# Optimization experiments

Hardware: AMD Instinct MI355X
Metric: run time of the kernel (lower is better)

The kernel has to match this reference:

```python
import jax, jax.numpy as jnp
import numpy as np

N, E, K, C, NB, G = 10000, 320000, 10, 32, 8, 8
RMAX, AVG = 5.0, 32.0
L_OF_M = np.array([0,1,1,1,2,2,2,2,2,3,3,3,3,3,3,3])
BLOCKS = [(0,1),(1,4),(4,9),(9,16)]


def _sph(u):
    # real spherical harmonics l=0..3, e3nn 'component' normalization (sum_m Y_lm^2 = 2l+1)
    x, y, z = u[:,0], u[:,1], u[:,2]
    s3=3**0.5; s5=5**0.5; s15=15**0.5; s105=105**0.5
    s35_8=(35.0/8.0)**0.5; s21_8=(21.0/8.0)**0.5; s7=7**0.5
    return jnp.stack([
        jnp.ones_like(x),
        s3*x, s3*y, s3*z,
        s15*x*y, s15*y*z, 0.5*s5*(3*z*z-1.0), s15*x*z, 0.5*s15*(x*x-y*y),
        s35_8*y*(3*x*x-y*y), s105*x*y*z, s21_8*y*(5*z*z-1.0),
        0.5*s7*z*(5*z*z-3.0), s21_8*x*(5*z*z-1.0), 0.5*s105*z*(x*x-y*y),
        s35_8*x*(x*x-3*y*y)], axis=-1)


def _radial(r):
    # Bessel basis * polynomial cutoff (p=5)
    n = jnp.arange(1, NB+1, dtype=r.dtype)
    bess = jnp.sqrt(2.0/RMAX)*jnp.sin(n*jnp.pi*r[:,None]/RMAX)/r[:,None]
    t = r/RMAX; p = 5.0
    env = 1.0 - (p+1)*(p+2)/2*t**5 + p*(p+2)*t**6 - p*(p+1)/2*t**7
    env = jnp.where(r < RMAX, env, 0.0)
    return bess*env[:,None]


def _interact(scal, ea, ef, snd, rcv, mws, Wl, n_nodes):
    h = ef
    for W in mws[:-1]:
        h = jax.nn.silu(h @ W)
    tw = (h @ mws[-1]).reshape(-1, C, 4)[:, :, L_OF_M]          # [E,C,16] per-(channel,l) tp weights
    mji = scal[snd][:, :, None] * tw * ea[:, None, :]            # per-edge CG-style tensor product
    msg = jax.ops.segment_sum(mji, rcv, num_segments=n_nodes) / AVG
    return jnp.concatenate([jnp.einsum('ncm,cd->ndm', msg[:, :, a:b], Wl[l])
                            for l, (a, b) in enumerate(BLOCKS)], axis=-1)


def _forward(positions, node_attrs, shifts, edge_index, batch, num_graphs,
             atomic_energies, W_emb, Wup1, M1a, M1b, M1c, M1d, Wl1, Wprod1,
             Wup2, M2a, M2b, M2c, M2d, Wl2, Wprod2, Wsc2, wr1, Wr2a, wr2b):
    snd, rcv = edge_index[0], edge_index[1]
    vec = positions[rcv] - positions[snd] + shifts
    r = jnp.sqrt(jnp.sum(vec*vec, -1) + 1e-12)
    ea = _sph(vec / r[:, None])           # [E,16]
    ef = _radial(r)                       # [E,8]
    nf0 = node_attrs @ W_emb              # node embedding [N,C]
    A1 = _interact(nf0 @ Wup1, ea, ef, snd, rcv, (M1a, M1b, M1c, M1d), Wl1, positions.shape[0])
    c1 = jnp.einsum('nk,kct->nct', node_attrs, Wprod1)          # element-dep product-basis coeffs
    a0 = A1[:, :, 0]
    nf1 = A1 * (c1[..., 0] + c1[..., 1]*a0 + c1[..., 2]*a0*a0)[:, :, None]  # correlation-3 product
    A2 = _interact(nf1[:, :, 0] @ Wup2, ea, ef, snd, rcv, (M2a, M2b, M2c, M2d), Wl2, positions.shape[0])
    pl = jnp.stack([jnp.sum(A2[:, :, a:b]**2, -1) for a, b in BLOCKS], -1)  # [N,C,4] invariants
    c2 = jnp.einsum('nk,kct->nct', node_attrs, Wprod2)
    nf2 = jnp.sum(c2*pl, -1) + jnp.einsum('nk,nc,kcd->nd', node_attrs, nf1[:, :, 0], Wsc2)
    e0 = node_attrs @ atomic_energies
    e1 = nf1[:, :, 0] @ wr1
    e2 = jax.nn.silu(nf2 @ Wr2a) @ wr2b
    node_energy = e0 + e1 + e2
    total = jax.ops.segment_sum(node_energy, batch, num_segments=num_graphs)
    return total, node_energy


def setup_inputs():
    key = jax.random.key(0)
    ks = jax.random.split(key, 24)
    s = 0.1
    inp = {}
    inp['positions'] = jax.random.normal(ks[0], (N, 3), jnp.float32)
    inp['node_attrs'] = jax.nn.one_hot(jax.random.randint(ks[1], (N,), 0, K), K, dtype=jnp.float32)
    inp['shifts'] = jnp.zeros((E, 3), jnp.float32)
    inp['edge_index'] = jax.random.randint(ks[2], (2, E), 0, N)
    inp['batch'] = jnp.sort(jax.random.randint(ks[3], (N,), 0, G))
    inp['num_graphs'] = G
    inp['atomic_energies'] = jax.random.normal(ks[4], (K,), jnp.float32)
    inp['W_emb'] = s*jax.random.normal(ks[5], (K, C), jnp.float32)
    inp['Wup1'] = s*jax.random.normal(ks[6], (C, C), jnp.float32)
    inp['M1a'] = s*jax.random.normal(ks[7], (NB, 64), jnp.float32)
    inp['M1b'] = s*jax.random.normal(ks[8], (64, 64), jnp.float32)
    inp['M1c'] = s*jax.random.normal(ks[9], (64, 64), jnp.float32)
    inp['M1d'] = s*jax.random.normal(ks[10], (64, C*4), jnp.float32)
    inp['Wl1'] = s*jax.random.normal(ks[11], (4, C, C), jnp.float32)
    inp['Wprod1'] = s*jax.random.normal(ks[12], (K, C, 3), jnp.float32)
    inp['Wup2'] = s*jax.random.normal(ks[13], (C, C), jnp.float32)
    inp['M2a'] = s*jax.random.normal(ks[14], (NB, 64), jnp.float32)
    inp['M2b'] = s*jax.random.normal(ks[15], (64, 64), jnp.float32)
    inp['M2c'] = s*jax.random.normal(ks[16], (64, 64), jnp.float32)
    inp['M2d'] = s*jax.random.normal(ks[17], (64, C*4), jnp.float32)
    inp['Wl2'] = s*jax.random.normal(ks[18], (4, C, C), jnp.float32)
    inp['Wprod2'] = s*jax.random.normal(ks[19], (K, C, 4), jnp.float32)
    inp['Wsc2'] = s*jax.random.normal(ks[20], (K, C, C), jnp.float32)
    inp['wr1'] = s*jax.random.normal(ks[21], (C,), jnp.float32)
    inp['Wr2a'] = s*jax.random.normal(ks[22], (C, 16), jnp.float32)
    inp['wr2b'] = s*jax.random.normal(ks[23], (16,), jnp.float32)
    return inp


def reference(positions, node_attrs, shifts, edge_index, batch, num_graphs,
              atomic_energies, W_emb, Wup1, M1a, M1b, M1c, M1d, Wl1, Wprod1,
              Wup2, M2a, M2b, M2c, M2d, Wl2, Wprod2, Wsc2, wr1, Wr2a, wr2b):
    def efn(pos):
        tot, ne = _forward(pos, node_attrs, shifts, edge_index, batch, num_graphs,
                           atomic_energies, W_emb, Wup1, M1a, M1b, M1c, M1d, Wl1, Wprod1,
                           Wup2, M2a, M2b, M2c, M2d, Wl2, Wprod2, Wsc2, wr1, Wr2a, wr2b)
        return jnp.sum(tot), (tot, ne)
    (_, (total, node_energy)), g = jax.value_and_grad(efn, has_aux=True)(positions)
    forces = -g  # forces = -dE/dpositions as in get_outputs
    return total, node_energy, forces
```

## Files before the change

### kernel.cpp

```cpp
#include <hip/hip_runtime.h>
#include <math.h>

#define NN 10000
#define NE 320000
#define KS 10
#define CC 32
#define GG 8
#define NTAB 2048
#define TROW 320
#define RMAXf 5.0f
#define AVGf 32.0f

#define OF_TAB 0
#define SZ_TAB ((NTAB + 1) * TROW)
#define OF_GEO (OF_TAB + SZ_TAB)
#define OF_SND (OF_GEO + 4 * NE)
#define OF_SPK (OF_SND + NE)
#define OF_RCSR (OF_SPK + NE)
#define OF_SC1 (OF_RCSR + NE)
#define OF_SP (OF_SC1 + KS * CC)
#define OF_RE (OF_SP + NN)
#define OF_UE (OF_RE + NE)
#define OF_GV (OF_UE + 3 * NE)
#define OF_A0 (OF_GV + 3 * NE)
#define OF_NF1 (OF_A0 + NN * CC)
#define OF_SCAL2 (OF_NF1 + NN * CC)
#define OF_NEP (OF_SCAL2 + NN * CC)
#define OF_GM2T (OF_NEP + NN)
#define OF_GNF1P (OF_GM2T + NN * CC * 16)
#define OF_GS1 (OF_GNF1P + NN * CC)
#define OF_ROWS (OF_GS1 + NN * CC)
#define OF_ELIST (OF_ROWS + NN + 1)
#define OF_DEG (OF_ELIST + NE)
#define OF_CUR (OF_DEG + NN)
#define OF_GSC2 (OF_CUR + NN)
#define OF_END (OF_GSC2 + NN * CC)

__device__ __forceinline__ int lm_of(int m) { return (m == 0) ? 0 : (m < 4) ? 1 : (m < 9) ? 2 : 3; }

__device__ __forceinline__ void sph16(float x, float y, float z, float* Y) {
    const float s3 = 1.7320508075688772f, s5 = 2.23606797749979f, s15 = 3.872983346207417f,
                s105 = 10.246950765959598f, s358 = 2.091650066335189f,
                s218 = 1.6201851746019651f, s7 = 2.6457513110645907f;
    Y[0] = 1.f;
    Y[1] = s3 * x; Y[2] = s3 * y; Y[3] = s3 * z;
    Y[4] = s15 * x * y; Y[5] = s15 * y * z; Y[6] = 0.5f * s5 * (3.f * z * z - 1.f);
    Y[7] = s15 * x * z; Y[8] = 0.5f * s15 * (x * x - y * y);
    Y[9] = s358 * y * (3.f * x * x - y * y);
    Y[10] = s105 * x * y * z;
    Y[11] = s218 * y * (5.f * z * z - 1.f);
    Y[12] = 0.5f * s7 * z * (5.f * z * z - 3.f);
    Y[13] = s218 * x * (5.f * z * z - 1.f);
    Y[14] = 0.5f * s105 * z * (x * x - y * y);
    Y[15] = s358 * x * (x * x - 3.f * y * y);
}

__device__ __forceinline__ void sph16_grad(float x, float y, float z, float* Dx, float* Dy, float* Dz) {
    const float s3 = 1.7320508075688772f, s5 = 2.23606797749979f, s15 = 3.872983346207417f,
                s105 = 10.246950765959598f, s358 = 2.091650066335189f,
                s218 = 1.6201851746019651f, s7 = 2.6457513110645907f;
    Dx[0] = 0; Dy[0] = 0; Dz[0] = 0;
    Dx[1] = s3; Dy[1] = 0; Dz[1] = 0;
    Dx[2] = 0; Dy[2] = s3; Dz[2] = 0;
    Dx[3] = 0; Dy[3] = 0; Dz[3] = s3;
    Dx[4] = s15 * y; Dy[4] = s15 * x; Dz[4] = 0;
    Dx[5] = 0; Dy[5] = s15 * z; Dz[5] = s15 * y;
    Dx[6] = 0; Dy[6] = 0; Dz[6] = 3.f * s5 * z;
    Dx[7] = s15 * z; Dy[7] = 0; Dz[7] = s15 * x;
    Dx[8] = s15 * x; Dy[8] = -s15 * y; Dz[8] = 0;
    Dx[9] = 6.f * s358 * x * y; Dy[9] = 3.f * s358 * (x * x - y * y); Dz[9] = 0;
    Dx[10] = s105 * y * z; Dy[10] = s105 * x * z; Dz[10] = s105 * x * y;
    Dx[11] = 0; Dy[11] = s218 * (5.f * z * z - 1.f); Dz[11] = 10.f * s218 * y * z;
    Dx[12] = 0; Dy[12] = 0; Dz[12] = 0.5f * s7 * (15.f * z * z - 3.f);
    Dx[13] = s218 * (5.f * z * z - 1.f); Dy[13] = 0; Dz[13] = 10.f * s218 * x * z;
    Dx[14] = s105 * x * z; Dy[14] = -s105 * y * z; Dz[14] = 0.5f * s105 * (x * x - y * y);
    Dx[15] = 3.f * s358 * (x * x - y * y); Dy[15] = -6.f * s358 * x * y; Dz[15] = 0;
}

__global__ void k_species(const float* __restrict__ na, int* __restrict__ sp) {
    int n = blockIdx.x * blockDim.x + threadIdx.x;
    if (n >= NN) return;
    int k = 0;
    for (int j = 0; j < KS; j++)
        if (na[n * KS + j] > 0.5f) k = j;
    sp[n] = k;
}

__global__ void k_scal1(const float* __restrict__ Wemb, const float* __restrict__ Wup1, float* __restrict__ st) {
    int i = threadIdx.x;
    if (i >= KS * CC) return;
    int k = i / CC, c = i % CC;
    float s = 0;
    for (int j = 0; j < CC; j++) s += Wemb[k * CC + j] * Wup1[j * CC + c];
    st[i] = s;
}

__global__ void k_table(const float* __restrict__ M1a, const float* __restrict__ M1b,
                        const float* __restrict__ M1c, const float* __restrict__ M1d,
                        const float* __restrict__ M2a, const float* __restrict__ M2b,
                        const float* __restrict__ M2c, const float* __restrict__ M2d,
                        float* __restrict__ tab) {
    const double PI = 3.14159265358979323846;
    int row = blockIdx.x;
    int j = threadIdx.x;
    __shared__ float sR[8], sdR[8];
    __shared__ float sA[64], sdA[64], sB[64], sdB[64];
    if (j < 8) {
        double r = (double)row * ((double)RMAXf / NTAB);
        if (r < 1e-6) r = 1e-6;
        double a = (double)(j + 1) * PI / (double)RMAXf;
        double env = 0.0, denv = 0.0;
        if (row < NTAB) {
            double t = r / (double)RMAXf;
            double t4 = t * t * t * t;
            env = 1.0 - 21.0 * t4 * t + 35.0 * t4 * t * t - 15.0 * t4 * t * t * t;
            denv = (-105.0 * t4 + 210.0 * t4 * t - 105.0 * t4 * t * t) / (double)RMAXf;
        }
        double pref = sqrt(2.0 / (double)RMAXf);
        double s = sin(a * r), cg = cos(a * r);
        double bess = pref * s / r;
        double dbess = pref * (a * cg / r - s / (r * r));
        sR[j] = (float)(bess * env);
        sdR[j] = (float)(dbess * env + bess * denv);
    }
    __syncthreads();
    size_t rb = (size_t)row * TROW;

    {
        float p = 0, dp = 0;
        for (int i = 0; i < 8; i++) { float w = M1a[i * 64 + j]; p += sR[i] * w; dp += sdR[i] * w; }
        float sg = 1.f / (1.f + expf(-p));
        sB[j] = p * sg; sdB[j] = dp * sg * (1.f + p * (1.f - sg));
    }
    __syncthreads();
    {
        float p = 0, dp = 0;
        for (int i = 0; i < 64; i++) { float w = M1b[i * 64 + j]; p += sB[i] * w; dp += sdB[i] * w; }
        float sg = 1.f / (1.f + expf(-p));
        sA[j] = p * sg; sdA[j] = dp * sg * (1.f + p * (1.f - sg));
    }
    __syncthreads();
    {
        float p = 0, dp = 0;
        for (int i = 0; i < 64; i++) { float w = M1c[i * 64 + j]; p += sA[i] * w; dp += sdA[i] * w; }
        float sg = 1.f / (1.f + expf(-p));
        sB[j] = p * sg; sdB[j] = dp * sg * (1.f + p * (1.f - sg));
    }
    __syncthreads();
    #pragma unroll
    for (int t2 = 0; t2 < 2; t2++) {
        int o = j + t2 * 64;
        if ((o & 3) == 0) {
            float p = 0, dp = 0;
            for (int i = 0; i < 64; i++) { float w = M1d[i * 128 + o]; p += sB[i] * w; dp += sdB[i] * w; }
            int c = o >> 2;
            tab[rb + c] = p;
            tab[rb + 32 + c] = dp;
        }
    }
    __syncthreads();

    {
        float p = 0, dp = 0;
        for (int i = 0; i < 8; i++) { float w = M2a[i * 64 + j]; p += sR[i] * w; dp += sdR[i] * w; }
        float sg = 1.f / (1.f + expf(-p));
        sB[j] = p * sg; sdB[j] = dp * sg * (1.f + p * (1.f - sg));
    }
    __syncthreads();
    {
        float p = 0, dp = 0;
        for (int i = 0; i < 64; i++) { float w = M2b[i * 64 + j]; p += sB[i] * w; dp += sdB[i] * w; }
        float sg = 1.f / (1.f + expf(-p));
        sA[j] = p * sg; sdA[j] = dp * sg * (1.f + p * (1.f - sg));
    }
    __syncthreads();
    {
        float p = 0, dp = 0;
        for (int i = 0; i < 64; i++) { float w = M2c[i * 64 + j]; p += sA[i] * w; dp += sdA[i] * w; }
        float sg = 1.f / (1.f + expf(-p));
        sB[j] = p * sg; sdB[j] = dp * sg * (1.f + p * (1.f - sg));
    }
    __syncthreads();
    #pragma unroll
    for (int t2 = 0; t2 < 2; t2++) {
        int o = j + t2 * 64;
        float p = 0, dp = 0;
        for (int i = 0; i < 64; i++) { float w = M2d[i * 128 + o]; p += sB[i] * w; dp += sdB[i] * w; }
        tab[rb + 64 + o] = p;
        tab[rb + 192 + o] = dp;
    }
}

__global__ void k_geom(const float* __restrict__ pos, const float* __restrict__ shifts,
                       const int* __restrict__ ei, float* __restrict__ re,
                       float* __restrict__ ue, int* __restrict__ deg) {
    int e = blockIdx.x * 256 + threadIdx.x;
    if (e >= NE) return;
    int s = ei[e], t = ei[NE + e];
    float vx = pos[3 * t] - pos[3 * s] + shifts[3 * e];
    float vy = pos[3 * t + 1] - pos[3 * s + 1] + shifts[3 * e + 1];
    float vz = pos[3 * t + 2] - pos[3 * s + 2] + shifts[3 * e + 2];
    float r = sqrtf(vx * vx + vy * vy + vz * vz + 1e-12f);
    float inv = 1.f / r;
    re[e] = r;
    ue[3 * e] = vx * inv;
    ue[3 * e + 1] = vy * inv;
    ue[3 * e + 2] = vz * inv;
    atomicAdd(&deg[t], 1);
}

__global__ void k_scan(const int* __restrict__ deg, int* __restrict__ rows, int* __restrict__ cur) {
    __shared__ int part[1024];
    int t = threadIdx.x;
    const int per = (NN + 1023) / 1024;
    int base = t * per;
    int s = 0;
    for (int i = 0; i < per; i++) {
        int idx = base + i;
        if (idx < NN) s += deg[idx];
    }
    part[t] = s;
    __syncthreads();
    for (int off = 1; off < 1024; off <<= 1) {
        int v = (t >= off) ? part[t - off] : 0;
        __syncthreads();
        part[t] += v;
        __syncthreads();
    }
    int run = (t == 0) ? 0 : part[t - 1];
    for (int i = 0; i < per; i++) {
        int idx = base + i;
        if (idx < NN) {
            rows[idx] = run;
            cur[idx] = run;
            run += deg[idx];
        }
    }
    if (t == 1023) rows[NN] = run;
}

__global__ void k_fill(const int* __restrict__ ei, const int* __restrict__ sp,
                       const float* __restrict__ re, const float* __restrict__ ue,
                       int* __restrict__ cur, int* __restrict__ elist,
                       int* __restrict__ snd, int* __restrict__ spk,
                       float* __restrict__ rcsr, float4* __restrict__ geo) {
    int e = blockIdx.x * 256 + threadIdx.x;
    if (e >= NE) return;
    int s = ei[e], t = ei[NE + e];
    int p = atomicAdd(&cur[t], 1);
    elist[p] = e;
    snd[p] = s;
    spk[p] = sp[s];
    rcsr[p] = re[e];
    geo[p] = make_float4(re[e], ue[3 * e], ue[3 * e + 1], ue[3 * e + 2]);
}

__global__ __launch_bounds__(256, 4)
void k_gather1(const int* __restrict__ rows, const int* __restrict__ spk,
               const float* __restrict__ rcsr, const int* __restrict__ sp,
               const float* __restrict__ sc1, const float* __restrict__ tab,
               const float* __restrict__ Wl1, const float* __restrict__ Wprod1,
               const float* __restrict__ Wup2, const float* __restrict__ wr1,
               const float* __restrict__ aE,
               float* __restrict__ a0s, float* __restrict__ nf1,
               float* __restrict__ scal2, float* __restrict__ nep) {
    __shared__ float red[4][CC];
    int wid = blockIdx.x;
    int tid = threadIdx.x;
    int wv = tid >> 6, lane = tid & 63, c = lane & 31, h = lane >> 5, hb = h << 5;
    int stream = wv * 2 + h;
    int r0 = rows[wid], dg = rows[wid + 1] - r0;
    float acc = 0.f;
    for (int j = stream; j < dg; j += 8) {
        int p = r0 + j;
        float r = rcsr[p];
        float scv = sc1[spk[p] * CC + c];
        float w1 = 0.f;
        if (r < RMAXf) {
            float tt = r * (NTAB / RMAXf);
            int i = (int)tt; if (i > NTAB - 1) i = NTAB - 1;
            float f = tt - (float)i;
            size_t b = (size_t)i * TROW + c;
            w1 = tab[b] * (1.f - f) + tab[b + TROW] * f;
        }
        acc += scv * w1;
    }
    acc += __shfl_xor(acc, 32, 64);
    if (h == 0) red[wv][c] = acc;
    __syncthreads();
    acc = red[0][c] + red[1][c] + red[2][c] + red[3][c];
    float a0 = 0.f;
    for (int d = 0; d < CC; d++) a0 += __shfl(acc, hb + d, 64) * Wl1[d * CC + c];
    a0 *= (1.f / AVGf);
    int k = sp[wid];
    const float* cp = &Wprod1[(k * CC + c) * 3];
    float nf = a0 * (cp[0] + cp[1] * a0 + cp[2] * a0 * a0);
    float s2 = 0.f;
    for (int d = 0; d < CC; d++) s2 += __shfl(nf, hb + d, 64) * Wup2[d * CC + c];
    float t1 = nf * wr1[c];
    for (int m = 16; m >= 1; m >>= 1) t1 += __shfl_xor(t1, m, 64);
    if (wv == 0 && h == 0) {
        a0s[wid * CC + c] = a0;
        nf1[wid * CC + c] = nf;
        scal2[wid * CC + c] = s2;
        if (c == 0) nep[wid] = aE[k] + t1;
    }
}

__global__ __launch_bounds__(256, 4)
void k_node2(const int* __restrict__ rows, const int* __restrict__ snd,
             const float4* __restrict__ geo, const int* __restrict__ sp,
             const float* __restrict__ scal2, const float* __restrict__ tab,
             const float* __restrict__ Wl2, const float* __restrict__ Wprod2,
             const float* __restrict__ Wsc2, const float* __restrict__ nf1,
             const float* __restrict__ Wr2a, const float* __restrict__ wr2b,
             const float* __restrict__ wr1, const float* __restrict__ nep,
             const int* __restrict__ batch,
             float* __restrict__ gm2T, float* __restrict__ gnf1p,
             float* __restrict__ out_total, float* __restrict__ out_ne) {
    __shared__ float lds[4][16 * 32];
    int wid = blockIdx.x;
    int tid = threadIdx.x;
    int wv = tid >> 6, lane = tid & 63, c = lane & 31, h = lane >> 5, hb = h << 5;
    int stream = wv * 2 + h;
    int r0 = rows[wid], dg = rows[wid + 1] - r0;

    float S2r[16];
    #pragma unroll
    for (int m = 0; m < 16; m++) S2r[m] = 0.f;
    for (int j = stream; j < dg; j += 8) {
        int p = r0 + j;
        float4 g4 = geo[p];
        float sc = scal2[snd[p] * CC + c];
        float r = g4.x;
        float scw[4] = {0, 0, 0, 0};
        if (r < RMAXf) {
            float tt = r * (NTAB / RMAXf);
            int i = (int)tt; if (i > NTAB - 1) i = NTAB - 1;
            float f = tt - (float)i;
            size_t b = (size_t)i * TROW + 64 + c * 4;
            float4 t0 = *(const float4*)&tab[b];
            float4 t1 = *(const float4*)&tab[b + TROW];
            scw[0] = sc * (t0.x + (t1.x - t0.x) * f);
            scw[1] = sc * (t0.y + (t1.y - t0.y) * f);
            scw[2] = sc * (t0.z + (t1.z - t0.z) * f);
            scw[3] = sc * (t0.w + (t1.w - t0.w) * f);
        }
        float Y[16];
        sph16(g4.y, g4.z, g4.w, Y);
        #pragma unroll
        for (int m = 0; m < 16; m++) S2r[m] += scw[lm_of(m)] * Y[m];
    }
    #pragma unroll
    for (int m = 0; m < 16; m++) S2r[m] += __shfl_xor(S2r[m], 32, 64);
    if (h == 0) {
        #pragma unroll
        for (int m = 0; m < 16; m++) lds[wv][m * 32 + c] = S2r[m];
    }
    __syncthreads();
    for (int idx = tid; idx < 512; idx += 256)
        lds[0][idx] += lds[1][idx] + lds[2][idx] + lds[3][idx];
    __syncthreads();

    int d = c;
    float A2r[16];
    #pragma unroll
    for (int m = 0; m < 16; m++) {
        const float* wl = &Wl2[lm_of(m) * CC * CC];
        float acc = 0;
        for (int cc = 0; cc < CC; cc++) acc += lds[0][m * 32 + cc] * wl[cc * CC + d];
        A2r[m] = acc * (1.f / AVGf);
    }
    float pl[4] = {0, 0, 0, 0};
    #pragma unroll
    for (int m = 0; m < 16; m++) pl[lm_of(m)] += A2r[m] * A2r[m];
    int k = sp[wid];
    const float* c2 = &Wprod2[(k * CC + d) * 4];
    float nf2 = c2[0] * pl[0] + c2[1] * pl[1] + c2[2] * pl[2] + c2[3] * pl[3];
    for (int cc = 0; cc < CC; cc++) nf2 += nf1[wid * CC + cc] * Wsc2[((size_t)k * CC + cc) * CC + d];
    int jj = d & 15;
    float zj = 0;
    for (int dd = 0; dd < CC; dd++) zj += __shfl(nf2, hb + dd, 64) * Wr2a[dd * 16 + jj];
    float sg = 1.f / (1.f + expf(-zj));
    float e2p = (d < 16) ? zj * sg * wr2b[jj] : 0.f;
    float red = e2p;
    for (int m = 16; m >= 1; m >>= 1) red += __shfl_xor(red, m, 64);
    if (wv == 0 && h == 0 && d == 0) {
        float ne = nep[wid] + red;
        out_ne[wid] = ne;
        atomicAdd(&out_total[batch[wid]], ne);
    }
    float gz = sg * (1.f + zj * (1.f - sg)) * wr2b[jj];
    float gn = 0;
    for (int j2 = 0; j2 < 16; j2++) gn += Wr2a[d * 16 + j2] * __shfl(gz, hb + j2, 64);
    __syncthreads();
    if (h == 0) {
        #pragma unroll
        for (int m = 0; m < 16; m++) lds[wv][m * 32 + d] = 2.f * A2r[m] * gn * c2[lm_of(m)];
    }
    __syncthreads();
    float gmv[16];
    #pragma unroll
    for (int m = 0; m < 16; m++) {
        const float* wl = &Wl2[lm_of(m) * CC * CC + c * CC];
        float acc = 0;
        for (int dd = 0; dd < CC; dd++) acc += lds[wv][m * 32 + dd] * wl[dd];
        gmv[m] = acc * (1.f / AVGf);
    }
    float g1 = wr1[c];
    for (int dd = 0; dd < CC; dd++) g1 += __shfl(gn, hb + dd, 64) * Wsc2[((size_t)k * CC + c) * CC + dd];
    if (wv == 0 && h == 0) {
        #pragma unroll
        for (int m = 0; m < 16; m++) gm2T[(size_t)wid * 512 + c * 16 + m] = gmv[m];
        gnf1p[wid * CC + c] = g1;
    }
}

__global__ __launch_bounds__(256, 4)
void k_gbwd2(const int* __restrict__ rows, const int* __restrict__ elist,
             const int* __restrict__ snd, const float4* __restrict__ geo,
             const float* __restrict__ scal2, const float* __restrict__ tab,
             const float* __restrict__ gm2T,
             float* __restrict__ gsc2, float* __restrict__ gvec) {
    int wid = blockIdx.x;
    int tid = threadIdx.x;
    int wv = tid >> 6, lane = tid & 63, c = lane & 31, h = lane >> 5;
    int stream = wv * 2 + h;
    float gm[16];
    #pragma unroll
    for (int m = 0; m < 16; m++) gm[m] = gm2T[(size_t)wid * 512 + c * 16 + m];
    int r0 = rows[wid], dg = rows[wid + 1] - r0;
    for (int j = stream; j < dg; j += 8) {
        int p = r0 + j;
        float4 g4 = geo[p];
        int s = snd[p];
        float sc = scal2[s * CC + c];
        float r = g4.x, ux = g4.y, uy = g4.z, uz = g4.w;
        float w2[4] = {0, 0, 0, 0}, scw[4] = {0, 0, 0, 0}, sdw[4] = {0, 0, 0, 0};
        if (r < RMAXf) {
            float tt = r * (NTAB / RMAXf);
            int i = (int)tt; if (i > NTAB - 1) i = NTAB - 1;
            float f = tt - (float)i;
            size_t b = (size_t)i * TROW + 64 + c * 4;
            size_t b2 = (size_t)i * TROW + 192 + c * 4;
            float4 t0 = *(const float4*)&tab[b];
            float4 t1 = *(const float4*)&tab[b + TROW];
            float4 d0 = *(const float4*)&tab[b2];
            float4 d1 = *(const float4*)&tab[b2 + TROW];
            w2[0] = t0.x + (t1.x - t0.x) * f; w2[1] = t0.y + (t1.y - t0.y) * f;
            w2[2] = t0.z + (t1.z - t0.z) * f; w2[3] = t0.w + (t1.w - t0.w) * f;
            sdw[0] = sc * (d0.x + (d1.x - d0.x) * f); sdw[1] = sc * (d0.y + (d1.y - d0.y) * f);
            sdw[2] = sc * (d0.z + (d1.z - d0.z) * f); sdw[3] = sc * (d0.w + (d1.w - d0.w) * f);
            scw[0] = sc * w2[0]; scw[1] = sc * w2[1]; scw[2] = sc * w2[2]; scw[3] = sc * w2[3];
        }
        float Y[16], Dx[16], Dy[16], Dz[16];
        sph16(ux, uy, uz, Y);
        sph16_grad(ux, uy, uz, Dx, Dy, Dz);
        float gsc = 0, gdr = 0, gx = 0, gy = 0, gz = 0;
        #pragma unroll
        for (int m = 0; m < 16; m++) {
            float g = gm[m];
            int l = lm_of(m);
            float t = g * Y[m];
            gsc += t * w2[l];
            gdr += t * sdw[l];
            float gY = g * scw[l];
            gx += gY * Dx[m]; gy += gY * Dy[m]; gz += gY * Dz[m];
        }
        atomicAdd(&gsc2[s * CC + c], gsc);
        for (int m2 = 16; m2 >= 1; m2 >>= 1) {
            gdr += __shfl_xor(gdr, m2, 64);
            gx += __shfl_xor(gx, m2, 64);
            gy += __shfl_xor(gy, m2, 64);
            gz += __shfl_xor(gz, m2, 64);
        }
        if (c == 0) {
            int e = elist[p];
            float inv = 1.f / r;
            float dot = ux * gx + uy * gy + uz * gz;
            gvec[3 * e] = ux * gdr + (gx - ux * dot) * inv;
            gvec[3 * e + 1] = uy * gdr + (gy - uy * dot) * inv;
            gvec[3 * e + 2] = uz * gdr + (gz - uz * dot) * inv;
        }
    }
}

__global__ void k_node_bwd2(const float* __restrict__ gnf1p, const float* __restrict__ gsc2,
                            const float* __restrict__ Wup2, const float* __restrict__ a0s,
                            const int* __restrict__ sp, const float* __restrict__ Wprod1,
                            const float* __restrict__ Wl1, float* __restrict__ gS1) {
    int gid = blockIdx.x * 256 + threadIdx.x;
    int n = gid >> 5, c = gid & 31;
    if (n >= NN) return;
    int hb = threadIdx.x & 32;
    float g1 = gnf1p[n * CC + c];
    for (int dd = 0; dd < CC; dd++) g1 += gsc2[n * CC + dd] * Wup2[c * CC + dd];
    float a0 = a0s[n * CC + c];
    int k = sp[n];
    const float* cp = &Wprod1[(k * CC + c) * 3];
    float ga0 = g1 * (cp[0] + 2.f * cp[1] * a0 + 3.f * cp[2] * a0 * a0);
    float acc = 0;
    for (int dd = 0; dd < CC; dd++) acc += __shfl(ga0, hb + dd, 64) * Wl1[c * CC + dd];
    gS1[n * CC + c] = acc * (1.f / AVGf);
}

__global__ void k_edge_bwd1(const int* __restrict__ ei, const int* __restrict__ sp,
                            const float* __restrict__ re, const float* __restrict__ ue,
                            const float* __restrict__ sc1, const float* __restrict__ tab,
                            const float* __restrict__ gS1, const float* __restrict__ gvec,
                            float* __restrict__ F) {
    int gid = blockIdx.x * 256 + threadIdx.x;
    int e = gid >> 5, c = gid & 31;
    if (e >= NE) return;
    int s = ei[e], t = ei[NE + e];
    float r = re[e];
    float dw = 0.f;
    if (r < RMAXf) {
        float tt = r * (NTAB / RMAXf);
        int i = (int)tt; if (i > NTAB - 1) i = NTAB - 1;
        float f = tt - (float)i;
        size_t b = (size_t)i * TROW + 32 + c;
        dw = tab[b] * (1.f - f) + tab[b + TROW] * f;
    }
    float gw = gS1[t * CC + c] * sc1[sp[s] * CC + c];
    float gdr = gw * dw;
    for (int m = 16; m >= 1; m >>= 1) gdr += __shfl_xor(gdr, m, 64);
    if (c < 3) {
        float u = ue[3 * e + c];
        float gv = gvec[3 * e + c] + u * gdr;
        atomicAdd(&F[3 * s + c], gv);
        atomicAdd(&F[3 * t + c], -gv);
    }
}

extern "C" void kernel_launch(void* const* d_in, const int* in_sizes, int n_in,
                              void* d_out, int out_size, void* d_ws, size_t ws_size,
                              hipStream_t stream) {
    const float* pos = (const float*)d_in[0];
    const float* na = (const float*)d_in[1];
    const float* shifts = (const float*)d_in[2];
    const int* ei = (const int*)d_in[3];
    const int* batch = (const int*)d_in[4];
    const float* aE = (const float*)d_in[6];
    const float* Wemb = (const float*)d_in[7];
    const float* Wup1 = (const float*)d_in[8];
    const float* M1a = (const float*)d_in[9];
    const float* M1b = (const float*)d_in[10];
    const float* M1c = (const float*)d_in[11];
    const float* M1d = (const float*)d_in[12];
    const float* Wl1 = (const float*)d_in[13];
    const float* Wprod1 = (const float*)d_in[14];
    const float* Wup2 = (const float*)d_in[15];
    const float* M2a = (const float*)d_in[16];
    const float* M2b = (const float*)d_in[17];
    const float* M2c = (const float*)d_in[18];
    const float* M2d = (const float*)d_in[19];
    const float* Wl2 = (const float*)d_in[20];
    const float* Wprod2 = (const float*)d_in[21];
    const float* Wsc2 = (const float*)d_in[22];
    const float* wr1 = (const float*)d_in[23];
    const float* Wr2a = (const float*)d_in[24];
    const float* wr2b = (const float*)d_in[25];

    float* ws = (float*)d_ws;
    float* tab = ws + OF_TAB;
    float4* geo = (float4*)(ws + OF_GEO);
    int* snd = (int*)(ws + OF_SND);
    int* spk = (int*)(ws + OF_SPK);
    float* rcsr = ws + OF_RCSR;
    float* sc1 = ws + OF_SC1;
    int* sp = (int*)(ws + OF_SP);
    float* re = ws + OF_RE;
    float* ue = ws + OF_UE;
    float* gv = ws + OF_GV;
    float* a0s = ws + OF_A0;
    float* nf1 = ws + OF_NF1;
    float* scal2 = ws + OF_SCAL2;
    float* nep = ws + OF_NEP;
    float* gm2T = ws + OF_GM2T;
    float* gnf1p = ws + OF_GNF1P;
    float* gS1 = ws + OF_GS1;
    int* rows = (int*)(ws + OF_ROWS);
    int* elist = (int*)(ws + OF_ELIST);
    int* deg = (int*)(ws + OF_DEG);
    int* cur = (int*)(ws + OF_CUR);
    float* gsc2 = ws + OF_GSC2;

    float* out_total = (float*)d_out;
    float* out_ne = out_total + GG;
    float* out_F = out_ne + NN;

    hipMemsetAsync(d_out, 0, sizeof(float) * (GG + NN + 3 * NN), stream);
    hipMemsetAsync(deg, 0, sizeof(float) * (size_t)(OF_END - OF_DEG), stream);

    k_species<<<(NN + 255) / 256, 256, 0, stream>>>(na, sp);
    k_scal1<<<1, 320, 0, stream>>>(Wemb, Wup1, sc1);
    k_table<<<NTAB + 1, 64, 0, stream>>>(M1a, M1b, M1c, M1d, M2a, M2b, M2c, M2d, tab);
    k_geom<<<(NE + 255) / 256, 256, 0, stream>>>(pos, shifts, ei, re, ue, deg);
    k_scan<<<1, 1024, 0, stream>>>(deg, rows, cur);
    k_fill<<<(NE + 255) / 256, 256, 0, stream>>>(ei, sp, re, ue, cur, elist, snd, spk, rcsr, geo);
    k_gather1<<<NN, 256, 0, stream>>>(rows, spk, rcsr, sp, sc1, tab, Wl1, Wprod1,
                                      Wup2, wr1, aE, a0s, nf1, scal2, nep);
    k_node2<<<NN, 256, 0, stream>>>(rows, snd, geo, sp, scal2, tab, Wl2,
                                    Wprod2, Wsc2, nf1, Wr2a, wr2b, wr1, nep, batch,
                                    gm2T, gnf1p, out_total, out_ne);
    k_gbwd2<<<NN, 256, 0, stream>>>(rows, elist, snd, geo, scal2, tab, gm2T, gsc2, gv);
    k_node_bwd2<<<NN / 8, 256, 0, stream>>>(gnf1p, gsc2, Wup2, a0s, sp, Wprod1, Wl1, gS1);
    k_edge_bwd1<<<NE / 8, 256, 0, stream>>>(ei, sp, re, ue, sc1, tab, gS1, gv, out_F);
}
```

Baseline: 468.2 us.

## Precompute spherical harmonics per CSR edge and move edge backward to receiver-grouped CSR

```diff
diff --git a/kernel.cpp b/kernel.cpp
--- a/kernel.cpp
+++ b/kernel.cpp
@@ -17,7 +17,8 @@
 #define OF_SND (OF_GEO + 4 * NE)
 #define OF_SPK (OF_SND + NE)
 #define OF_RCSR (OF_SPK + NE)
-#define OF_SC1 (OF_RCSR + NE)
+#define OF_YE (OF_RCSR + NE)
+#define OF_SC1 (OF_YE + 16 * NE)
 #define OF_SP (OF_SC1 + KS * CC)
 #define OF_RE (OF_SP + NN)
 #define OF_UE (OF_RE + NE)
@@ -30,8 +31,7 @@
 #define OF_GNF1P (OF_GM2T + NN * CC * 16)
 #define OF_GS1 (OF_GNF1P + NN * CC)
 #define OF_ROWS (OF_GS1 + NN * CC)
-#define OF_ELIST (OF_ROWS + NN + 1)
-#define OF_DEG (OF_ELIST + NE)
+#define OF_DEG (OF_ROWS + NN + 1)
 #define OF_CUR (OF_DEG + NN)
 #define OF_GSC2 (OF_CUR + NN)
 #define OF_END (OF_GSC2 + NN * CC)
@@ -241,18 +241,25 @@
 
 __global__ void k_fill(const int* __restrict__ ei, const int* __restrict__ sp,
                        const float* __restrict__ re, const float* __restrict__ ue,
-                       int* __restrict__ cur, int* __restrict__ elist,
-                       int* __restrict__ snd, int* __restrict__ spk,
-                       float* __restrict__ rcsr, float4* __restrict__ geo) {
+                       int* __restrict__ cur, int* __restrict__ snd, int* __restrict__ spk,
+                       float* __restrict__ rcsr, float4* __restrict__ geo,
+                       float* __restrict__ YE) {
     int e = blockIdx.x * 256 + threadIdx.x;
     if (e >= NE) return;
     int s = ei[e], t = ei[NE + e];
     int p = atomicAdd(&cur[t], 1);
-    elist[p] = e;
+    float ux = ue[3 * e], uy = ue[3 * e + 1], uz = ue[3 * e + 2];
     snd[p] = s;
     spk[p] = sp[s];
     rcsr[p] = re[e];
-    geo[p] = make_float4(re[e], ue[3 * e], ue[3 * e + 1], ue[3 * e + 2]);
+    geo[p] = make_float4(re[e], ux, uy, uz);
+    float Y[16];
+    sph16(ux, uy, uz, Y);
+    float4* yp = (float4*)&YE[(size_t)p * 16];
+    yp[0] = make_float4(Y[0], Y[1], Y[2], Y[3]);
+    yp[1] = make_float4(Y[4], Y[5], Y[6], Y[7]);
+    yp[2] = make_float4(Y[8], Y[9], Y[10], Y[11]);
+    yp[3] = make_float4(Y[12], Y[13], Y[14], Y[15]);
 }
 
 __global__ __launch_bounds__(256, 4)
@@ -288,6 +295,7 @@
     acc += __shfl_xor(acc, 32, 64);
     if (h == 0) red[wv][c] = acc;
     __syncthreads();
+    if (wv != 0) return;
     acc = red[0][c] + red[1][c] + red[2][c] + red[3][c];
     float a0 = 0.f;
     for (int d = 0; d < CC; d++) a0 += __shfl(acc, hb + d, 64) * Wl1[d * CC + c];
@@ -299,7 +307,7 @@
     for (int d = 0; d < CC; d++) s2 += __shfl(nf, hb + d, 64) * Wup2[d * CC + c];
     float t1 = nf * wr1[c];
     for (int m = 16; m >= 1; m >>= 1) t1 += __shfl_xor(t1, m, 64);
-    if (wv == 0 && h == 0) {
+    if (h == 0) {
         a0s[wid * CC + c] = a0;
         nf1[wid * CC + c] = nf;
         scal2[wid * CC + c] = s2;
@@ -309,7 +317,8 @@
 
 __global__ __launch_bounds__(256, 4)
 void k_node2(const int* __restrict__ rows, const int* __restrict__ snd,
-             const float4* __restrict__ geo, const int* __restrict__ sp,
+             const float* __restrict__ rcsr, const float* __restrict__ YE,
+             const int* __restrict__ sp,
              const float* __restrict__ scal2, const float* __restrict__ tab,
              const float* __restrict__ Wl2, const float* __restrict__ Wprod2,
              const float* __restrict__ Wsc2, const float* __restrict__ nf1,
@@ -330,9 +339,8 @@
     for (int m = 0; m < 16; m++) S2r[m] = 0.f;
     for (int j = stream; j < dg; j += 8) {
         int p = r0 + j;
-        float4 g4 = geo[p];
+        float r = rcsr[p];
         float sc = scal2[snd[p] * CC + c];
-        float r = g4.x;
         float scw[4] = {0, 0, 0, 0};
         if (r < RMAXf) {
             float tt = r * (NTAB / RMAXf);
@@ -346,8 +354,10 @@
             scw[2] = sc * (t0.z + (t1.z - t0.z) * f);
             scw[3] = sc * (t0.w + (t1.w - t0.w) * f);
         }
-        float Y[16];
-        sph16(g4.y, g4.z, g4.w, Y);
+        const float4* yp = (const float4*)&YE[(size_t)p * 16];
+        float4 y0 = yp[0], y1 = yp[1], y2 = yp[2], y3 = yp[3];
+        float Y[16] = {y0.x, y0.y, y0.z, y0.w, y1.x, y1.y, y1.z, y1.w,
+                       y2.x, y2.y, y2.z, y2.w, y3.x, y3.y, y3.z, y3.w};
         #pragma unroll
         for (int m = 0; m < 16; m++) S2r[m] += scw[lm_of(m)] * Y[m];
     }
@@ -361,6 +371,7 @@
     for (int idx = tid; idx < 512; idx += 256)
         lds[0][idx] += lds[1][idx] + lds[2][idx] + lds[3][idx];
     __syncthreads();
+    if (wv != 0) return;
 
     int d = c;
     float A2r[16];
@@ -385,7 +396,7 @@
     float e2p = (d < 16) ? zj * sg * wr2b[jj] : 0.f;
     float red = e2p;
     for (int m = 16; m >= 1; m >>= 1) red += __shfl_xor(red, m, 64);
-    if (wv == 0 && h == 0 && d == 0) {
+    if (h == 0 && d == 0) {
         float ne = nep[wid] + red;
         out_ne[wid] = ne;
         atomicAdd(&out_total[batch[wid]], ne);
@@ -393,23 +404,21 @@
     float gz = sg * (1.f + zj * (1.f - sg)) * wr2b[jj];
     float gn = 0;
     for (int j2 = 0; j2 < 16; j2++) gn += Wr2a[d * 16 + j2] * __shfl(gz, hb + j2, 64);
-    __syncthreads();
     if (h == 0) {
         #pragma unroll
-        for (int m = 0; m < 16; m++) lds[wv][m * 32 + d] = 2.f * A2r[m] * gn * c2[lm_of(m)];
-    }
-    __syncthreads();
+        for (int m = 0; m < 16; m++) lds[0][m * 32 + d] = 2.f * A2r[m] * gn * c2[lm_of(m)];
+    }
     float gmv[16];
     #pragma unroll
     for (int m = 0; m < 16; m++) {
         const float* wl = &Wl2[lm_of(m) * CC * CC + c * CC];
         float acc = 0;
-        for (int dd = 0; dd < CC; dd++) acc += lds[wv][m * 32 + dd] * wl[dd];
+        for (int dd = 0; dd < CC; dd++) acc += lds[0][m * 32 + dd] * wl[dd];
         gmv[m] = acc * (1.f / AVGf);
     }
     float g1 = wr1[c];
     for (int dd = 0; dd < CC; dd++) g1 += __shfl(gn, hb + dd, 64) * Wsc2[((size_t)k * CC + c) * CC + dd];
-    if (wv == 0 && h == 0) {
+    if (h == 0) {
         #pragma unroll
         for (int m = 0; m < 16; m++) gm2T[(size_t)wid * 512 + c * 16 + m] = gmv[m];
         gnf1p[wid * CC + c] = g1;
@@ -417,11 +426,11 @@
 }
 
 __global__ __launch_bounds__(256, 4)
-void k_gbwd2(const int* __restrict__ rows, const int* __restrict__ elist,
-             const int* __restrict__ snd, const float4* __restrict__ geo,
+void k_gbwd2(const int* __restrict__ rows, const int* __restrict__ snd,
+             const float4* __restrict__ geo, const float* __restrict__ YE,
              const float* __restrict__ scal2, const float* __restrict__ tab,
              const float* __restrict__ gm2T,
-             float* __restrict__ gsc2, float* __restrict__ gvec) {
+             float* __restrict__ gsc2, float* __restrict__ gvcsr) {
     int wid = blockIdx.x;
     int tid = threadIdx.x;
     int wv = tid >> 6, lane = tid & 63, c = lane & 31, h = lane >> 5;
@@ -453,8 +462,11 @@
             sdw[2] = sc * (d0.z + (d1.z - d0.z) * f); sdw[3] = sc * (d0.w + (d1.w - d0.w) * f);
             scw[0] = sc * w2[0]; scw[1] = sc * w2[1]; scw[2] = sc * w2[2]; scw[3] = sc * w2[3];
         }
-        float Y[16], Dx[16], Dy[16], Dz[16];
-        sph16(ux, uy, uz, Y);
+        const float4* yp = (const float4*)&YE[(size_t)p * 16];
+        float4 y0 = yp[0], y1 = yp[1], y2 = yp[2], y3 = yp[3];
+        float Y[16] = {y0.x, y0.y, y0.z, y0.w, y1.x, y1.y, y1.z, y1.w,
+                       y2.x, y2.y, y2.z, y2.w, y3.x, y3.y, y3.z, y3.w};
+        float Dx[16], Dy[16], Dz[16];
         sph16_grad(ux, uy, uz, Dx, Dy, Dz);
         float gsc = 0, gdr = 0, gx = 0, gy = 0, gz = 0;
         #pragma unroll
@@ -475,12 +487,11 @@
             gz += __shfl_xor(gz, m2, 64);
         }
         if (c == 0) {
-            int e = elist[p];
             float inv = 1.f / r;
             float dot = ux * gx + uy * gy + uz * gz;
-            gvec[3 * e] = ux * gdr + (gx - ux * dot) * inv;
-            gvec[3 * e + 1] = uy * gdr + (gy - uy * dot) * inv;
-            gvec[3 * e + 2] = uz * gdr + (gz - uz * dot) * inv;
+            gvcsr[3 * p] = ux * gdr + (gx - ux * dot) * inv;
+            gvcsr[3 * p + 1] = uy * gdr + (gy - uy * dot) * inv;
+            gvcsr[3 * p + 2] = uz * gdr + (gz - uz * dot) * inv;
         }
     }
 }
@@ -504,33 +515,42 @@
     gS1[n * CC + c] = acc * (1.f / AVGf);
 }
 
-__global__ void k_edge_bwd1(const int* __restrict__ ei, const int* __restrict__ sp,
-                            const float* __restrict__ re, const float* __restrict__ ue,
-                            const float* __restrict__ sc1, const float* __restrict__ tab,
-                            const float* __restrict__ gS1, const float* __restrict__ gvec,
-                            float* __restrict__ F) {
-    int gid = blockIdx.x * 256 + threadIdx.x;
-    int e = gid >> 5, c = gid & 31;
-    if (e >= NE) return;
-    int s = ei[e], t = ei[NE + e];
-    float r = re[e];
-    float dw = 0.f;
-    if (r < RMAXf) {
-        float tt = r * (NTAB / RMAXf);
-        int i = (int)tt; if (i > NTAB - 1) i = NTAB - 1;
-        float f = tt - (float)i;
-        size_t b = (size_t)i * TROW + 32 + c;
-        dw = tab[b] * (1.f - f) + tab[b + TROW] * f;
-    }
-    float gw = gS1[t * CC + c] * sc1[sp[s] * CC + c];
-    float gdr = gw * dw;
-    for (int m = 16; m >= 1; m >>= 1) gdr += __shfl_xor(gdr, m, 64);
-    if (c < 3) {
-        float u = ue[3 * e + c];
-        float gv = gvec[3 * e + c] + u * gdr;
-        atomicAdd(&F[3 * s + c], gv);
-        atomicAdd(&F[3 * t + c], -gv);
-    }
+__global__ __launch_bounds__(256, 4)
+void k_gbwd1(const int* __restrict__ rows, const int* __restrict__ snd,
+             const int* __restrict__ spk, const float* __restrict__ rcsr,
+             const float4* __restrict__ geo, const float* __restrict__ sc1,
+             const float* __restrict__ tab, const float* __restrict__ gS1,
+             const float* __restrict__ gvcsr, float* __restrict__ F) {
+    int wid = blockIdx.x;
+    int tid = threadIdx.x;
+    int wv = tid >> 6, lane = tid & 63, c = lane & 31, h = lane >> 5;
+    int stream = wv * 2 + h;
+    int r0 = rows[wid], dg = rows[wid + 1] - r0;
+    float gst = gS1[wid * CC + c];
+    float ft = 0.f;
+    for (int j = stream; j < dg; j += 8) {
+        int p = r0 + j;
+        float r = rcsr[p];
+        int s = snd[p];
+        float dw = 0.f;
+        if (r < RMAXf) {
+            float tt = r * (NTAB / RMAXf);
+            int i = (int)tt; if (i > NTAB - 1) i = NTAB - 1;
+            float f = tt - (float)i;
+            size_t b = (size_t)i * TROW + 32 + c;
+            dw = tab[b] * (1.f - f) + tab[b + TROW] * f;
+        }
+        float gdr = gst * sc1[spk[p] * CC + c] * dw;
+        for (int m = 16; m >= 1; m >>= 1) gdr += __shfl_xor(gdr, m, 64);
+        if (c < 3) {
+            float4 g4 = geo[p];
+            float u = (c == 0) ? g4.y : (c == 1) ? g4.z : g4.w;
+            float gv = gvcsr[3 * p + c] + u * gdr;
+            atomicAdd(&F[3 * s + c], gv);
+            ft -= gv;
+        }
+    }
+    if (c < 3) atomicAdd(&F[3 * wid + c], ft);
 }
 
 extern "C" void kernel_launch(void* const* d_in, const int* in_sizes, int n_in,
@@ -568,6 +588,7 @@
     int* snd = (int*)(ws + OF_SND);
     int* spk = (int*)(ws + OF_SPK);
     float* rcsr = ws + OF_RCSR;
+    float* YE = ws + OF_YE;
     float* sc1 = ws + OF_SC1;
     int* sp = (int*)(ws + OF_SP);
     float* re = ws + OF_RE;
@@ -581,7 +602,6 @@
     float* gnf1p = ws + OF_GNF1P;
     float* gS1 = ws + OF_GS1;
     int* rows = (int*)(ws + OF_ROWS);
-    int* elist = (int*)(ws + OF_ELIST);
     int* deg = (int*)(ws + OF_DEG);
     int* cur = (int*)(ws + OF_CUR);
     float* gsc2 = ws + OF_GSC2;
@@ -598,13 +618,13 @@
     k_table<<<NTAB + 1, 64, 0, stream>>>(M1a, M1b, M1c, M1d, M2a, M2b, M2c, M2d, tab);
     k_geom<<<(NE + 255) / 256, 256, 0, stream>>>(pos, shifts, ei, re, ue, deg);
     k_scan<<<1, 1024, 0, stream>>>(deg, rows, cur);
-    k_fill<<<(NE + 255) / 256, 256, 0, stream>>>(ei, sp, re, ue, cur, elist, snd, spk, rcsr, geo);
+    k_fill<<<(NE + 255) / 256, 256, 0, stream>>>(ei, sp, re, ue, cur, snd, spk, rcsr, geo, YE);
     k_gather1<<<NN, 256, 0, stream>>>(rows, spk, rcsr, sp, sc1, tab, Wl1, Wprod1,
                                       Wup2, wr1, aE, a0s, nf1, scal2, nep);
-    k_node2<<<NN, 256, 0, stream>>>(rows, snd, geo, sp, scal2, tab, Wl2,
+    k_node2<<<NN, 256, 0, stream>>>(rows, snd, rcsr, YE, sp, scal2, tab, Wl2,
                                     Wprod2, Wsc2, nf1, Wr2a, wr2b, wr1, nep, batch,
                                     gm2T, gnf1p, out_total, out_ne);
-    k_gbwd2<<<NN, 256, 0, stream>>>(rows, elist, snd, geo, scal2, tab, gm2T, gsc2, gv);
+    k_gbwd2<<<NN, 256, 0, stream>>>(rows, snd, geo, YE, scal2, tab, gm2T, gsc2, gv);
     k_node_bwd2<<<NN / 8, 256, 0, stream>>>(gnf1p, gsc2, Wup2, a0s, sp, Wprod1, Wl1, gS1);
-    k_edge_bwd1<<<NE / 8, 256, 0, stream>>>(ei, sp, re, ue, sc1, tab, gS1, gv, out_F);
-}
+    k_gbwd1<<<NN, 256, 0, stream>>>(rows, snd, spk, rcsr, geo, sc1, tab, gS1, gv, out_F);
+}
```

New measurement: 440.2 us. -6.0%, faster.
